# Kernel tuning notes

Hardware: AMD Instinct MI355X
Metric: run time of the kernel (lower is better)

## Reference

```python
import jax, jax.numpy as jnp
import numpy as np

N = 100000   # nodes
E = 1600000  # edges
G = 512      # graphs
L = 3        # num_unit LEConv layers
D = 64       # hidden dim


def setup_inputs() -> dict:
    key = jax.random.key(0)
    ks = jax.random.split(key, 12)
    s = 1.0 / np.sqrt(D)
    x = jax.random.normal(ks[0], (N, 4), jnp.float32)
    edge_index = jax.random.randint(ks[1], (2, E), 0, N, dtype=jnp.int64)
    edge_attr = jax.random.uniform(ks[2], (E,), jnp.float32)
    batch = jnp.sort(jax.random.randint(ks[3], (N,), 0, G, dtype=jnp.int64))
    return {
        "x": x,
        "edge_index": edge_index,
        "edge_attr": edge_attr,
        "batch": batch,
        "W_emb": jax.random.normal(ks[4], (4, D), jnp.float32) * 0.5,
        "b_emb": jnp.zeros((D,), jnp.float32),
        "W1": jax.random.normal(ks[5], (L, D, D), jnp.float32) * s,  # LEConv lin1 (on x_j)
        "b1": jnp.zeros((L, D), jnp.float32),
        "W2": jax.random.normal(ks[6], (L, D, D), jnp.float32) * s,  # LEConv lin2 (on x_i, no bias)
        "W3": jax.random.normal(ks[7], (L, D, D), jnp.float32) * s,  # LEConv lin3 (root)
        "b3": jnp.zeros((L, D), jnp.float32),
        "Wl1": jax.random.normal(ks[8], (D, 32), jnp.float32) * s,
        "bl1": jnp.zeros((32,), jnp.float32),
        "Wl2": jax.random.normal(ks[9], (32, 3), jnp.float32) * (1.0 / np.sqrt(32)),
        "bl2": jnp.zeros((3,), jnp.float32),
    }


def reference(x, edge_index, edge_attr, batch, W_emb, b_emb,
              W1, b1, W2, W3, b3, Wl1, bl1, Wl2, bl2):
    src, dst = edge_index[0], edge_index[1]
    h = x @ W_emb + b_emb                          # [N, D]
    for l in range(L):
        a = h @ W1[l] + b1[l]                      # lin1(x) -> gathered at source j
        b = h @ W2[l]                              # lin2(x) -> gathered at target i
        # LEConv message: e_ij * (lin1(x_j) - lin2(x_i)), aggr='add' at target
        msg = edge_attr[:, None] * (a[src] - b[dst])   # [E, D]
        agg = jax.ops.segment_sum(msg, dst, num_segments=N)
        h = jax.nn.relu(agg + h @ W3[l] + b3[l])
    # global_mean_pool over graphs
    sums = jax.ops.segment_sum(h, batch, num_segments=G)              # [G, D]
    counts = jax.ops.segment_sum(jnp.ones((N,), h.dtype), batch, num_segments=G)
    graph_x = sums / jnp.maximum(counts, 1.0)[:, None]
    pred = jax.nn.relu(graph_x @ Wl1 + bl1) @ Wl2 + bl2               # [G, 3]
    return pred
```

## Files before the change

### kernel.cpp

```cpp
#include <hip/hip_runtime.h>
#include <hip/hip_bf16.h>

#define NNODES 100000
#define NEDGES 1600000
#define NGRAPH 512
#define DIM    64
#define NLAYER 3

#define NB   1000
#define BN   100
#define CAP  2048
#define SC_BLOCKS 256
#define EPB  6250
#define PACK_BLOCKS 18

typedef __attribute__((ext_vector_type(8))) short short8;
typedef __attribute__((ext_vector_type(4))) float float4v;
typedef unsigned long long u64;

__device__ __forceinline__ float b2f(__hip_bfloat16 v) { return __bfloat162float(v); }
__device__ __forceinline__ __hip_bfloat16 f2b(float f) { return __float2bfloat16(f); }
__device__ __forceinline__ unsigned short f2b_bits(float f) {
    __hip_bfloat16 h = __float2bfloat16(f);
    return *reinterpret_cast<unsigned short*>(&h);
}

__device__ __forceinline__ unsigned pack_rec(int src, unsigned wbits32) {
    unsigned w15 = ((wbits32 + 0x8000u) >> 16) & 0x7FFFu;
    return ((unsigned)src << 15) | w15;
}

#define ACC4(ACC, RR, VV) do {                                              \
    float _w = __uint_as_float(((RR) & 0x7FFFu) << 16);                     \
    unsigned _lo = (unsigned)(VV), _hi = (unsigned)((VV) >> 32);            \
    ACC[0] = fmaf(_w, __uint_as_float(_lo << 16), ACC[0]);                  \
    ACC[1] = fmaf(_w, __uint_as_float(_lo & 0xFFFF0000u), ACC[1]);          \
    ACC[2] = fmaf(_w, __uint_as_float(_hi << 16), ACC[2]);                  \
    ACC[3] = fmaf(_w, __uint_as_float(_hi & 0xFFFF0000u), ACC[3]);          \
} while (0)


__global__ __launch_bounds__(256) void local_sort_kernel(
    const int* __restrict__ ei, const float* __restrict__ ea,
    int2* __restrict__ perm_raw, int2* __restrict__ offcnt,
    const float* __restrict__ W1, const float* __restrict__ W2,
    const float* __restrict__ W3, __hip_bfloat16* __restrict__ wpack) {
    int tid = threadIdx.x, k = blockIdx.x;
    if (k >= SC_BLOCKS) {
        int unit = (k - SC_BLOCKS) * 4 + (tid >> 6);
        if (unit < NLAYER * 24) {
            int kh = unit & 1, tn = (unit >> 1) & 3, w = (unit >> 3) % 3, l = unit / 24;
            const float* Wsrc = (w == 0 ? W1 : (w == 1 ? W2 : W3)) + l * 4096;
            int L = tid & 63;
            __hip_bfloat16* dst = wpack + (size_t)unit * 512 + L * 8;
            int kb = 32 * kh + (L >> 4) * 8;
            int nb = 16 * tn + (L & 15);
            #pragma unroll
            for (int j = 0; j < 8; ++j)
                dst[j] = f2b(Wsrc[(kb + j) * 64 + nb]);
        }
        return;
    }
    __shared__ int cnt[NB];
    __shared__ int off[NB];
    __shared__ int partial[256];
    __shared__ int2 srec[EPB];
    int e0 = k * EPB;
    for (int i = tid; i < NB; i += 256) cnt[i] = 0;
    __syncthreads();
    for (int i = tid; i < EPB; i += 256)
        atomicAdd(&cnt[ei[NEDGES + e0 + i] / BN], 1);
    __syncthreads();
    int loc[4]; int s = 0;
    #pragma unroll
    for (int j = 0; j < 4; ++j) {
        int b = tid * 4 + j;
        int v = (b < NB) ? cnt[b] : 0;
        loc[j] = s; s += v;
    }
    partial[tid] = s;
    __syncthreads();
    for (int o = 1; o < 256; o <<= 1) {
        int t = (tid >= o) ? partial[tid - o] : 0;
        __syncthreads();
        partial[tid] += t;
        __syncthreads();
    }
    int excl = partial[tid] - s;
    #pragma unroll
    for (int j = 0; j < 4; ++j) {
        int b = tid * 4 + j;
        if (b < NB) off[b] = excl + loc[j];
    }
    __syncthreads();
    for (int b = tid; b < NB; b += 256)
        offcnt[(size_t)k * NB + b] = make_int2(off[b], cnt[b]);
    __syncthreads();
    for (int i = tid; i < EPB; i += 256) {
        int e = e0 + i;
        int src = ei[e];
        int d = ei[NEDGES + e];
        float w = ea[e];
        int bin = d / BN;
        int dloc = d - bin * BN;
        int pos = atomicAdd(&off[bin], 1);
        srec[pos] = make_int2(src | (dloc << 20), __float_as_int(w));
    }
    __syncthreads();
    for (int i = tid; i < EPB; i += 256)
        perm_raw[e0 + i] = srec[i];
}

__global__ __launch_bounds__(256) void bucket_csr_kernel(
    const int2* __restrict__ perm_raw, const int2* __restrict__ offcnt,
    unsigned* __restrict__ perm2, int2* __restrict__ rows, float* __restrict__ wdeg) {
    __shared__ int2     recs[CAP];
    __shared__ unsigned recs2u[CAP];
    __shared__ int   pscan[256];
    __shared__ int   sprefix[SC_BLOCKS + 1];
    __shared__ int   boff[SC_BLOCKS];
    __shared__ int   cnt[BN];
    __shared__ int   start[BN];
    __shared__ int   cur[BN];
    __shared__ float ws[BN];
    int b = blockIdx.x, tid = threadIdx.x;
    if (tid < BN) { cnt[tid] = 0; ws[tid] = 0.f; }
    int2 oc = offcnt[(size_t)tid * NB + b];
    boff[tid] = oc.x;
    int c = oc.y;
    pscan[tid] = c;
    __syncthreads();
    for (int o = 1; o < 256; o <<= 1) {
        int t = (tid >= o) ? pscan[tid - o] : 0;
        __syncthreads();
        pscan[tid] += t;
        __syncthreads();
    }
    sprefix[tid] = pscan[tid] - c;
    if (tid == 255) sprefix[256] = pscan[255];
    __syncthreads();
    int n = min(sprefix[SC_BLOCKS], CAP);
    for (int i = tid; i < n; i += 256) {
        int lo = 0, hi = SC_BLOCKS;
        while (hi - lo > 1) { int m = (lo + hi) >> 1; if (sprefix[m] <= i) lo = m; else hi = m; }
        int2 rec = perm_raw[lo * EPB + boff[lo] + (i - sprefix[lo])];
        recs[i] = rec;
        atomicAdd(&cnt[rec.x >> 20], 1);
        atomicAdd(&ws[rec.x >> 20], __int_as_float(rec.y));
    }
    __syncthreads();
    {
        int v = (tid < BN) ? cnt[tid] : 0;
        pscan[tid] = v;
        __syncthreads();
        for (int o = 1; o < 128; o <<= 1) {
            int t = (tid >= o) ? pscan[tid - o] : 0;
            __syncthreads();
            pscan[tid] += t;
            __syncthreads();
        }
        if (tid < BN) start[tid] = pscan[tid] - v;
    }
    __syncthreads();
    if (tid < BN) {
        cur[tid] = start[tid];
        int base = b * CAP + start[tid];
        rows[b * BN + tid] = make_int2(base, base + cnt[tid]);
        wdeg[b * BN + tid] = ws[tid];
    }
    __syncthreads();
    for (int i = tid; i < n; i += 256) {
        int2 rec = recs[i];
        int pos = atomicAdd(&cur[rec.x >> 20], 1);
        recs2u[pos] = pack_rec(rec.x & 0xFFFFF, (unsigned)rec.y);
    }
    __syncthreads();
    for (int i = tid; i < n; i += 256)
        perm2[(size_t)b * CAP + i] = recs2u[i];
}


template <int FUSE_EMBED>
__global__ __launch_bounds__(256) void gemm3_mfma_kernel(
    __hip_bfloat16* __restrict__ h16, const float* __restrict__ wdeg,
    const __hip_bfloat16* __restrict__ wpack,
    const float* __restrict__ b1, const float* __restrict__ b3,
    __hip_bfloat16* __restrict__ a,
    const float* __restrict__ x, const float* __restrict__ Wemb,
    const float* __restrict__ bemb) {
    int tid = threadIdx.x;
    int lane = tid & 63, wv = tid >> 6;
    int m0 = blockIdx.x * 64 + wv * 16;
    int q = lane >> 4;
    int node_a = m0 + (lane & 15);
    int node_c = min(node_a, NNODES - 1);

    float4v acc[3][4] = {};
    const short8* wp = (const short8*)wpack;

    float4v xv;
    if (FUSE_EMBED) xv = *(const float4v*)&x[(size_t)node_c * 4];

    #pragma unroll
    for (int kh = 0; kh < 2; ++kh) {
        short8 afrag;
        if (FUSE_EMBED) {
            #pragma unroll
            for (int j = 0; j < 8; ++j) {
                int ch = kh * 32 + q * 8 + j;
                float s = bemb[ch];
                #pragma unroll
                for (int k = 0; k < 4; ++k) s = fmaf(xv[k], Wemb[k * 64 + ch], s);
                afrag[j] = (short)f2b_bits(s);
            }
        } else {
            afrag = *(const short8*)((const short*)h16 + (size_t)node_c * 64 + kh * 32 + q * 8);
        }
        #pragma unroll
        for (int w = 0; w < 3; ++w) {
            #pragma unroll
            for (int tn = 0; tn < 4; ++tn) {
                short8 bfrag = wp[(size_t)(((w * 4 + tn) * 2 + kh)) * 64 + lane];
                acc[w][tn] = __builtin_amdgcn_mfma_f32_16x16x32_bf16(afrag, bfrag, acc[w][tn], 0, 0, 0);
            }
        }
    }

    int coll = lane & 15;
    float b1v[4], b3v[4];
    #pragma unroll
    for (int tn = 0; tn < 4; ++tn) {
        b1v[tn] = b1[tn * 16 + coll];
        b3v[tn] = b3[tn * 16 + coll];
    }
    #pragma unroll
    for (int reg = 0; reg < 4; ++reg) {
        int node = m0 + q * 4 + reg;
        if (node < NNODES) {
            float wd = wdeg[node];
            #pragma unroll
            for (int tn = 0; tn < 4; ++tn) {
                int nn = tn * 16 + coll;
                a[(size_t)node * 64 + nn] = f2b(acc[0][tn][reg] + b1v[tn]);
                h16[(size_t)node * 64 + nn] = f2b(acc[2][tn][reg] + b3v[tn] - wd * acc[1][tn][reg]);
            }
        }
    }
}

__global__ __launch_bounds__(256) void edge_agg_kernel(
    const __hip_bfloat16* __restrict__ a, __hip_bfloat16* __restrict__ h16,
    const int2* __restrict__ rows, const unsigned* __restrict__ perm2) {
    int node = blockIdx.x * 4 + (threadIdx.x >> 6);
    int lane = threadIdx.x & 63;
    int q = lane >> 4, p = lane & 15;
    const u64* a64 = (const u64*)a;
    int2 r = rows[node];
    int start = r.x, end = r.y;
    u64 cv = 0;
    if (q == 0) cv = ((const u64*)h16)[(size_t)node * 16 + p];
    float accA[4] = {0.f, 0.f, 0.f, 0.f};
    float accB[4] = {0.f, 0.f, 0.f, 0.f};
    float accC[4] = {0.f, 0.f, 0.f, 0.f};
    float accD[4] = {0.f, 0.f, 0.f, 0.f};
    for (int cb = start; cb < end; cb += 64) {
        int avail = end - cb;
        int cnt = min(avail, 64);
        unsigned rec = (lane < avail) ? perm2[cb + lane] : 0u;
        int full = cnt >> 4;
        for (int t = 0; t < full; ++t) {
            int base = t * 16;
            unsigned rA = (unsigned)__shfl((int)rec, base + q, 64);
            unsigned rB = (unsigned)__shfl((int)rec, base + 4 + q, 64);
            unsigned rC = (unsigned)__shfl((int)rec, base + 8 + q, 64);
            unsigned rD = (unsigned)__shfl((int)rec, base + 12 + q, 64);
            u64 vA = a64[(size_t)(rA >> 15) * 16 + p];
            u64 vB = a64[(size_t)(rB >> 15) * 16 + p];
            u64 vC = a64[(size_t)(rC >> 15) * 16 + p];
            u64 vD = a64[(size_t)(rD >> 15) * 16 + p];
            ACC4(accA, rA, vA);
            ACC4(accB, rB, vB);
            ACC4(accC, rC, vC);
            ACC4(accD, rD, vD);
        }
        int rem = cnt & 15;
        if (rem) {
            int base = full << 4;
            unsigned rA = (unsigned)__shfl((int)rec, base + q, 64);
            u64 vA = a64[(size_t)(rA >> 15) * 16 + p];
            unsigned rB = 0u, rC = 0u, rD = 0u;
            u64 vB = 0, vC = 0, vD = 0;
            if (rem > 4) {
                rB = (unsigned)__shfl((int)rec, base + 4 + q, 64);
                vB = a64[(size_t)(rB >> 15) * 16 + p];
            }
            if (rem > 8) {
                rC = (unsigned)__shfl((int)rec, base + 8 + q, 64);
                vC = a64[(size_t)(rC >> 15) * 16 + p];
            }
            if (rem > 12) {
                rD = (unsigned)__shfl((int)rec, base + 12 + q, 64);
                vD = a64[(size_t)(rD >> 15) * 16 + p];
            }
            ACC4(accA, rA, vA);
            ACC4(accB, rB, vB);
            ACC4(accC, rC, vC);
            ACC4(accD, rD, vD);
        }
    }
    #pragma unroll
    for (int j = 0; j < 4; ++j) accA[j] = (accA[j] + accB[j]) + (accC[j] + accD[j]);
    #pragma unroll
    for (int j = 0; j < 4; ++j) accA[j] += __shfl_xor(accA[j], 16, 64);
    #pragma unroll
    for (int j = 0; j < 4; ++j) accA[j] += __shfl_xor(accA[j], 32, 64);
    if (q == 0) {
        u64* h64 = (u64*)h16;
        unsigned int lo = (unsigned int)cv, hi = (unsigned int)(cv >> 32);
        float r0 = fmaxf(__uint_as_float(lo << 16) + accA[0], 0.f);
        float r1 = fmaxf(__uint_as_float(lo & 0xFFFF0000u) + accA[1], 0.f);
        float r2 = fmaxf(__uint_as_float(hi << 16) + accA[2], 0.f);
        float r3 = fmaxf(__uint_as_float(hi & 0xFFFF0000u) + accA[3], 0.f);
        u64 outv = (u64)f2b_bits(r0) | ((u64)f2b_bits(r1) << 16) |
                   ((u64)f2b_bits(r2) << 32) | ((u64)f2b_bits(r3) << 48);
        h64[(size_t)node * 16 + p] = outv;
    }
}


__global__ __launch_bounds__(256) void pool_mlp_kernel(
    const __hip_bfloat16* __restrict__ h16, const int* __restrict__ batch,
    const float* __restrict__ Wl1, const float* __restrict__ bl1,
    const float* __restrict__ Wl2, const float* __restrict__ bl2,
    float* __restrict__ out) {
    __shared__ int lohi[2];
    __shared__ float red[16][64];
    __shared__ float gxl[64];
    __shared__ float hid[32];
    int g = blockIdx.x;
    int tid = threadIdx.x;
    if (tid < 2) {
        int target = g + tid;
        int lo = 0, hi = NNODES;
        while (lo < hi) { int m = (lo + hi) >> 1; if (batch[m] < target) lo = m + 1; else hi = m; }
        lohi[tid] = lo;
    }
    __syncthreads();
    int lo = lohi[0], hi = lohi[1];
    int grp = tid >> 4, p = tid & 15;
    float s0 = 0.f, s1 = 0.f, s2 = 0.f, s3 = 0.f;
    const u64* h64 = (const u64*)h16;
    for (int n = lo + grp; n < hi; n += 16) {
        u64 v = h64[(size_t)n * 16 + p];
        unsigned lo32 = (unsigned)v, hi32 = (unsigned)(v >> 32);
        s0 += __uint_as_float(lo32 << 16);
        s1 += __uint_as_float(lo32 & 0xFFFF0000u);
        s2 += __uint_as_float(hi32 << 16);
        s3 += __uint_as_float(hi32 & 0xFFFF0000u);
    }
    float4v sv = {s0, s1, s2, s3};
    *(float4v*)&red[grp][p * 4] = sv;
    __syncthreads();
    if (tid < 64) {
        float tot = 0.f;
        #pragma unroll
        for (int k = 0; k < 16; ++k) tot += red[k][tid];
        int cnt = hi - lo;
        gxl[tid] = tot / (float)max(cnt, 1);
    }
    __syncthreads();
    if (tid < 32) {
        float s = bl1[tid];
        for (int k = 0; k < 64; ++k) s = fmaf(gxl[k], Wl1[k * 32 + tid], s);
        hid[tid] = fmaxf(s, 0.f);
    }
    __syncthreads();
    if (tid < 3) {
        float s = bl2[tid];
        for (int k = 0; k < 32; ++k) s = fmaf(hid[k], Wl2[k * 3 + tid], s);
        out[g * 3 + tid] = s;
    }
}


extern "C" void kernel_launch(void* const* d_in, const int* in_sizes, int n_in,
                              void* d_out, int out_size, void* d_ws, size_t ws_size,
                              hipStream_t stream) {
    const float* x    = (const float*)d_in[0];
    const int*   ei   = (const int*)d_in[1];
    const float* ea   = (const float*)d_in[2];
    const int*   bat  = (const int*)d_in[3];
    const float* Wemb = (const float*)d_in[4];
    const float* bemb = (const float*)d_in[5];
    const float* W1   = (const float*)d_in[6];
    const float* b1   = (const float*)d_in[7];
    const float* W2   = (const float*)d_in[8];
    const float* W3   = (const float*)d_in[9];
    const float* b3   = (const float*)d_in[10];
    const float* Wl1  = (const float*)d_in[11];
    const float* bl1  = (const float*)d_in[12];
    const float* Wl2  = (const float*)d_in[13];
    const float* bl2  = (const float*)d_in[14];
    float* out = (float*)d_out;

    char* ws = (char*)d_ws;
    __hip_bfloat16*  a        = (__hip_bfloat16*) (ws + 0);
    __hip_bfloat16*  h16      = (__hip_bfloat16*) (ws + 12800000);
    int2*            perm_raw = (int2*)           (ws + 25600000);
    unsigned*        perm2    = (unsigned*)       (ws + 38400000);
    int2*            rows     = (int2*)           (ws + 46592000);
    int2*            offcnt   = (int2*)           (ws + 47392000);
    float*           wdeg     = (float*)          (ws + 49440000);
    __hip_bfloat16*  wpack    = (__hip_bfloat16*) (ws + 49840000);

    local_sort_kernel<<<SC_BLOCKS + PACK_BLOCKS, 256, 0, stream>>>(
        ei, ea, perm_raw, offcnt, W1, W2, W3, wpack);
    bucket_csr_kernel<<<NB, 256, 0, stream>>>(perm_raw, offcnt, perm2, rows, wdeg);

    gemm3_mfma_kernel<1><<<(NNODES + 63) / 64, 256, 0, stream>>>(
        h16, wdeg, wpack, b1, b3, a, x, Wemb, bemb);
    edge_agg_kernel<<<NNODES / 4, 256, 0, stream>>>(a, h16, rows, perm2);
    for (int l = 1; l < NLAYER; ++l) {
        gemm3_mfma_kernel<0><<<(NNODES + 63) / 64, 256, 0, stream>>>(
            h16, wdeg, wpack + (size_t)l * 24 * 512, b1 + l * 64, b3 + l * 64, a,
            x, Wemb, bemb);
        edge_agg_kernel<<<NNODES / 4, 256, 0, stream>>>(a, h16, rows, perm2);
    }
    pool_mlp_kernel<<<NGRAPH, 256, 0, stream>>>(h16, bat, Wl1, bl1, Wl2, bl2, out);
}
```

Measured before the change: 293.6 us.

## Aggregate raw h before the GEMM and fuse each layer into one kernel

Uses linearity to reorder each layer: the edge-weighted sum of neighbour h is gathered first, and W1 is applied to that sum (with the bias scaled by weighted degree) inside one fused gather+MFMA kernel per layer. The separate a-buffer write/read and the per-layer two-kernel split go away, and h is ping-ponged between two buffers. The last layer also reduces into per-graph sums with atomics, replacing the pooling pass, so the final MLP kernel only reads the sums. This adds atomics and a next-node record prefetch. It also changes rounding order, since the aggregate is rounded to bf16 before the GEMM.

```diff
diff --git a/kernel.cpp b/kernel.cpp
--- a/kernel.cpp
+++ b/kernel.cpp
@@ -13,12 +13,13 @@
 #define SC_BLOCKS 256
 #define EPB  6250
 #define PACK_BLOCKS 18
+#define ZERO_BLOCKS 2
+#define NBLK 1563
 
 typedef __attribute__((ext_vector_type(8))) short short8;
 typedef __attribute__((ext_vector_type(4))) float float4v;
 typedef unsigned long long u64;
 
-__device__ __forceinline__ float b2f(__hip_bfloat16 v) { return __bfloat162float(v); }
 __device__ __forceinline__ __hip_bfloat16 f2b(float f) { return __float2bfloat16(f); }
 __device__ __forceinline__ unsigned short f2b_bits(float f) {
     __hip_bfloat16 h = __float2bfloat16(f);
@@ -39,13 +40,66 @@
     ACC[3] = fmaf(_w, __uint_as_float(_hi & 0xFFFF0000u), ACC[3]);          \
 } while (0)
 
+__device__ __forceinline__ void gather_rounds(
+    unsigned rec, int cnt, const u64* __restrict__ h64, int q, int p,
+    float (&accA)[4], float (&accB)[4], float (&accC)[4], float (&accD)[4]) {
+    int full = cnt >> 4;
+    for (int t = 0; t < full; ++t) {
+        int base = t * 16;
+        unsigned rA = (unsigned)__shfl((int)rec, base + q, 64);
+        unsigned rB = (unsigned)__shfl((int)rec, base + 4 + q, 64);
+        unsigned rC = (unsigned)__shfl((int)rec, base + 8 + q, 64);
+        unsigned rD = (unsigned)__shfl((int)rec, base + 12 + q, 64);
+        u64 vA = h64[(size_t)(rA >> 15) * 16 + p];
+        u64 vB = h64[(size_t)(rB >> 15) * 16 + p];
+        u64 vC = h64[(size_t)(rC >> 15) * 16 + p];
+        u64 vD = h64[(size_t)(rD >> 15) * 16 + p];
+        ACC4(accA, rA, vA);
+        ACC4(accB, rB, vB);
+        ACC4(accC, rC, vC);
+        ACC4(accD, rD, vD);
+    }
+    int rem = cnt & 15;
+    if (rem) {
+        int base = full << 4;
+        unsigned rA = (unsigned)__shfl((int)rec, base + q, 64);
+        u64 vA = h64[(size_t)(rA >> 15) * 16 + p];
+        unsigned rB = 0u, rC = 0u, rD = 0u;
+        u64 vB = 0, vC = 0, vD = 0;
+        if (rem > 4) {
+            rB = (unsigned)__shfl((int)rec, base + 4 + q, 64);
+            vB = h64[(size_t)(rB >> 15) * 16 + p];
+        }
+        if (rem > 8) {
+            rC = (unsigned)__shfl((int)rec, base + 8 + q, 64);
+            vC = h64[(size_t)(rC >> 15) * 16 + p];
+        }
+        if (rem > 12) {
+            rD = (unsigned)__shfl((int)rec, base + 12 + q, 64);
+            vD = h64[(size_t)(rD >> 15) * 16 + p];
+        }
+        ACC4(accA, rA, vA);
+        ACC4(accB, rB, vB);
+        ACC4(accC, rC, vC);
+        ACC4(accD, rD, vD);
+    }
+}
+
 
 __global__ __launch_bounds__(256) void local_sort_kernel(
     const int* __restrict__ ei, const float* __restrict__ ea,
     int2* __restrict__ perm_raw, int2* __restrict__ offcnt,
     const float* __restrict__ W1, const float* __restrict__ W2,
-    const float* __restrict__ W3, __hip_bfloat16* __restrict__ wpack) {
+    const float* __restrict__ W3, __hip_bfloat16* __restrict__ wpack,
+    float* __restrict__ gsum) {
     int tid = threadIdx.x, k = blockIdx.x;
+    if (k >= SC_BLOCKS + PACK_BLOCKS) {
+        float4v z = {0.f, 0.f, 0.f, 0.f};
+        int idx = (k - SC_BLOCKS - PACK_BLOCKS) * 256 + tid;
+        for (int i = idx; i < NGRAPH * DIM / 4; i += ZERO_BLOCKS * 256)
+            ((float4v*)gsum)[i] = z;
+        return;
+    }
     if (k >= SC_BLOCKS) {
         int unit = (k - SC_BLOCKS) * 4 + (tid >> 6);
         if (unit < NLAYER * 24) {
@@ -180,205 +234,181 @@
 }
 
 
-template <int FUSE_EMBED>
-__global__ __launch_bounds__(256) void gemm3_mfma_kernel(
-    __hip_bfloat16* __restrict__ h16, const float* __restrict__ wdeg,
-    const __hip_bfloat16* __restrict__ wpack,
+__global__ __launch_bounds__(256) void embed_kernel(
+    const float* __restrict__ x, const float* __restrict__ Wemb,
+    const float* __restrict__ bemb, __hip_bfloat16* __restrict__ h) {
+    int t = blockIdx.x * 256 + threadIdx.x;
+    int node = t >> 4, d0 = (t & 15) * 4;
+    if (node >= NNODES) return;
+    float4v xv = *(const float4v*)&x[(size_t)node * 4];
+    u64 w0 = 0;
+    #pragma unroll
+    for (int j = 0; j < 4; ++j) {
+        int ch = d0 + j;
+        float s = bemb[ch];
+        #pragma unroll
+        for (int k = 0; k < 4; ++k) s = fmaf(xv[k], Wemb[k * 64 + ch], s);
+        w0 |= (u64)f2b_bits(s) << (16 * j);
+    }
+    ((u64*)h)[(size_t)node * 16 + (t & 15)] = w0;
+}
+
+
+template <int LAST>
+__global__ __launch_bounds__(256) void layer_kernel(
+    const __hip_bfloat16* __restrict__ hin, __hip_bfloat16* __restrict__ hout,
+    const int2* __restrict__ rows, const unsigned* __restrict__ perm2,
+    const float* __restrict__ wdeg, const __hip_bfloat16* __restrict__ wpack,
     const float* __restrict__ b1, const float* __restrict__ b3,
-    __hip_bfloat16* __restrict__ a,
-    const float* __restrict__ x, const float* __restrict__ Wemb,
-    const float* __restrict__ bemb) {
+    const int* __restrict__ batch, float* __restrict__ gsum) {
+    __shared__ __align__(16) unsigned char mbytes[4 * 2048];
     int tid = threadIdx.x;
     int lane = tid & 63, wv = tid >> 6;
-    int m0 = blockIdx.x * 64 + wv * 16;
-    int q = lane >> 4;
-    int node_a = m0 + (lane & 15);
-    int node_c = min(node_a, NNODES - 1);
+    int q = lane >> 4, p = lane & 15;
+    int m0w = blockIdx.x * 64 + wv * 16;
+    const u64* h64 = (const u64*)hin;
+
+    int2 rall = rows[min(m0w + p, NNODES - 1)];
+    int st_n = __shfl(rall.x, 0, 64);
+    int en_n = __shfl(rall.y, 0, 64);
+    if (m0w >= NNODES) en_n = st_n;
+    unsigned rec_n = (lane < min(en_n - st_n, 64)) ? perm2[st_n + lane] : 0u;
+
+    for (int nl = 0; nl < 16; ++nl) {
+        int st = st_n, en = en_n;
+        unsigned rec = rec_n;
+        if (nl < 15) {
+            st_n = __shfl(rall.x, nl + 1, 64);
+            en_n = __shfl(rall.y, nl + 1, 64);
+            if (m0w + nl + 1 >= NNODES) en_n = st_n;
+            rec_n = (lane < min(en_n - st_n, 64)) ? perm2[st_n + lane] : 0u;
+        }
+        float accA[4] = {0.f, 0.f, 0.f, 0.f};
+        float accB[4] = {0.f, 0.f, 0.f, 0.f};
+        float accC[4] = {0.f, 0.f, 0.f, 0.f};
+        float accD[4] = {0.f, 0.f, 0.f, 0.f};
+        gather_rounds(rec, min(en - st, 64), h64, q, p, accA, accB, accC, accD);
+        for (int cb = st + 64; cb < en; cb += 64) {
+            unsigned rec2 = (lane < en - cb) ? perm2[cb + lane] : 0u;
+            gather_rounds(rec2, min(en - cb, 64), h64, q, p, accA, accB, accC, accD);
+        }
+        #pragma unroll
+        for (int j = 0; j < 4; ++j) accA[j] = (accA[j] + accB[j]) + (accC[j] + accD[j]);
+        #pragma unroll
+        for (int j = 0; j < 4; ++j) accA[j] += __shfl_xor(accA[j], 16, 64);
+        #pragma unroll
+        for (int j = 0; j < 4; ++j) accA[j] += __shfl_xor(accA[j], 32, 64);
+        if (q == 0) {
+            u64 w0 = (u64)f2b_bits(accA[0]) | ((u64)f2b_bits(accA[1]) << 16) |
+                     ((u64)f2b_bits(accA[2]) << 32) | ((u64)f2b_bits(accA[3]) << 48);
+            int off = (wv * 2048 + nl * 128 + p * 8) ^ ((nl & 7) << 4);
+            *(u64*)(mbytes + off) = w0;
+        }
+    }
 
     float4v acc[3][4] = {};
     const short8* wp = (const short8*)wpack;
-
-    float4v xv;
-    if (FUSE_EMBED) xv = *(const float4v*)&x[(size_t)node_c * 4];
-
+    int node_c = min(m0w + p, NNODES - 1);
     #pragma unroll
     for (int kh = 0; kh < 2; ++kh) {
-        short8 afrag;
-        if (FUSE_EMBED) {
-            #pragma unroll
-            for (int j = 0; j < 8; ++j) {
-                int ch = kh * 32 + q * 8 + j;
-                float s = bemb[ch];
-                #pragma unroll
-                for (int k = 0; k < 4; ++k) s = fmaf(xv[k], Wemb[k * 64 + ch], s);
-                afrag[j] = (short)f2b_bits(s);
-            }
-        } else {
-            afrag = *(const short8*)((const short*)h16 + (size_t)node_c * 64 + kh * 32 + q * 8);
-        }
+        int roff = (wv * 2048 + p * 128 + kh * 64 + q * 16) ^ ((p & 7) << 4);
+        short8 am = *(const short8*)(mbytes + roff);
+        short8 ah = *(const short8*)((const short*)hin + (size_t)node_c * 64 + kh * 32 + q * 8);
         #pragma unroll
         for (int w = 0; w < 3; ++w) {
             #pragma unroll
             for (int tn = 0; tn < 4; ++tn) {
-                short8 bfrag = wp[(size_t)(((w * 4 + tn) * 2 + kh)) * 64 + lane];
-                acc[w][tn] = __builtin_amdgcn_mfma_f32_16x16x32_bf16(afrag, bfrag, acc[w][tn], 0, 0, 0);
+                short8 bfrag = wp[(size_t)((w * 4 + tn) * 2 + kh) * 64 + lane];
+                acc[w][tn] = __builtin_amdgcn_mfma_f32_16x16x32_bf16(
+                    w == 0 ? am : ah, bfrag, acc[w][tn], 0, 0, 0);
             }
         }
     }
 
-    int coll = lane & 15;
     float b1v[4], b3v[4];
     #pragma unroll
     for (int tn = 0; tn < 4; ++tn) {
-        b1v[tn] = b1[tn * 16 + coll];
-        b3v[tn] = b3[tn * 16 + coll];
-    }
-    #pragma unroll
-    for (int reg = 0; reg < 4; ++reg) {
-        int node = m0 + q * 4 + reg;
-        if (node < NNODES) {
-            float wd = wdeg[node];
+        b1v[tn] = b1[tn * 16 + p];
+        b3v[tn] = b3[tn * 16 + p];
+    }
+    if (!LAST) {
+        #pragma unroll
+        for (int reg = 0; reg < 4; ++reg) {
+            int node = m0w + q * 4 + reg;
+            if (node < NNODES) {
+                float wd = wdeg[node];
+                #pragma unroll
+                for (int tn = 0; tn < 4; ++tn) {
+                    float s = acc[0][tn][reg] + acc[2][tn][reg] + b3v[tn] +
+                              wd * (b1v[tn] - acc[1][tn][reg]);
+                    hout[(size_t)node * 64 + tn * 16 + p] = f2b(fmaxf(s, 0.f));
+                }
+            }
+        }
+    } else {
+        float val[4][4];
+        int gb[4];
+        #pragma unroll
+        for (int reg = 0; reg < 4; ++reg) {
+            int node = m0w + q * 4 + reg;
+            int nc = min(node, NNODES - 1);
+            float wd = wdeg[nc];
+            gb[reg] = batch[nc];
+            bool ok = node < NNODES;
             #pragma unroll
             for (int tn = 0; tn < 4; ++tn) {
-                int nn = tn * 16 + coll;
-                a[(size_t)node * 64 + nn] = f2b(acc[0][tn][reg] + b1v[tn]);
-                h16[(size_t)node * 64 + nn] = f2b(acc[2][tn][reg] + b3v[tn] - wd * acc[1][tn][reg]);
+                float s = acc[0][tn][reg] + acc[2][tn][reg] + b3v[tn] +
+                          wd * (b1v[tn] - acc[1][tn][reg]);
+                val[reg][tn] = ok ? fmaxf(s, 0.f) : 0.f;
             }
         }
-    }
-}
-
-__global__ __launch_bounds__(256) void edge_agg_kernel(
-    const __hip_bfloat16* __restrict__ a, __hip_bfloat16* __restrict__ h16,
-    const int2* __restrict__ rows, const unsigned* __restrict__ perm2) {
-    int node = blockIdx.x * 4 + (threadIdx.x >> 6);
-    int lane = threadIdx.x & 63;
-    int q = lane >> 4, p = lane & 15;
-    const u64* a64 = (const u64*)a;
-    int2 r = rows[node];
-    int start = r.x, end = r.y;
-    u64 cv = 0;
-    if (q == 0) cv = ((const u64*)h16)[(size_t)node * 16 + p];
-    float accA[4] = {0.f, 0.f, 0.f, 0.f};
-    float accB[4] = {0.f, 0.f, 0.f, 0.f};
-    float accC[4] = {0.f, 0.f, 0.f, 0.f};
-    float accD[4] = {0.f, 0.f, 0.f, 0.f};
-    for (int cb = start; cb < end; cb += 64) {
-        int avail = end - cb;
-        int cnt = min(avail, 64);
-        unsigned rec = (lane < avail) ? perm2[cb + lane] : 0u;
-        int full = cnt >> 4;
-        for (int t = 0; t < full; ++t) {
-            int base = t * 16;
-            unsigned rA = (unsigned)__shfl((int)rec, base + q, 64);
-            unsigned rB = (unsigned)__shfl((int)rec, base + 4 + q, 64);
-            unsigned rC = (unsigned)__shfl((int)rec, base + 8 + q, 64);
-            unsigned rD = (unsigned)__shfl((int)rec, base + 12 + q, 64);
-            u64 vA = a64[(size_t)(rA >> 15) * 16 + p];
-            u64 vB = a64[(size_t)(rB >> 15) * 16 + p];
-            u64 vC = a64[(size_t)(rC >> 15) * 16 + p];
-            u64 vD = a64[(size_t)(rD >> 15) * 16 + p];
-            ACC4(accA, rA, vA);
-            ACC4(accB, rB, vB);
-            ACC4(accC, rC, vC);
-            ACC4(accD, rD, vD);
-        }
-        int rem = cnt & 15;
-        if (rem) {
-            int base = full << 4;
-            unsigned rA = (unsigned)__shfl((int)rec, base + q, 64);
-            u64 vA = a64[(size_t)(rA >> 15) * 16 + p];
-            unsigned rB = 0u, rC = 0u, rD = 0u;
-            u64 vB = 0, vC = 0, vD = 0;
-            if (rem > 4) {
-                rB = (unsigned)__shfl((int)rec, base + 4 + q, 64);
-                vB = a64[(size_t)(rB >> 15) * 16 + p];
+        int glo = batch[min(m0w, NNODES - 1)];
+        int ghi = batch[min(m0w + 15, NNODES - 1)];
+        for (int g = glo; g <= ghi; ++g) {
+            #pragma unroll
+            for (int tn = 0; tn < 4; ++tn) {
+                float part = 0.f;
+                #pragma unroll
+                for (int reg = 0; reg < 4; ++reg)
+                    part += (gb[reg] == g) ? val[reg][tn] : 0.f;
+                part += __shfl_xor(part, 16, 64);
+                part += __shfl_xor(part, 32, 64);
+                if (q == 0) atomicAdd(&gsum[g * 64 + tn * 16 + p], part);
             }
-            if (rem > 8) {
-                rC = (unsigned)__shfl((int)rec, base + 8 + q, 64);
-                vC = a64[(size_t)(rC >> 15) * 16 + p];
-            }
-            if (rem > 12) {
-                rD = (unsigned)__shfl((int)rec, base + 12 + q, 64);
-                vD = a64[(size_t)(rD >> 15) * 16 + p];
-            }
-            ACC4(accA, rA, vA);
-            ACC4(accB, rB, vB);
-            ACC4(accC, rC, vC);
-            ACC4(accD, rD, vD);
-        }
-    }
-    #pragma unroll
-    for (int j = 0; j < 4; ++j) accA[j] = (accA[j] + accB[j]) + (accC[j] + accD[j]);
-    #pragma unroll
-    for (int j = 0; j < 4; ++j) accA[j] += __shfl_xor(accA[j], 16, 64);
-    #pragma unroll
-    for (int j = 0; j < 4; ++j) accA[j] += __shfl_xor(accA[j], 32, 64);
-    if (q == 0) {
-        u64* h64 = (u64*)h16;
-        unsigned int lo = (unsigned int)cv, hi = (unsigned int)(cv >> 32);
-        float r0 = fmaxf(__uint_as_float(lo << 16) + accA[0], 0.f);
-        float r1 = fmaxf(__uint_as_float(lo & 0xFFFF0000u) + accA[1], 0.f);
-        float r2 = fmaxf(__uint_as_float(hi << 16) + accA[2], 0.f);
-        float r3 = fmaxf(__uint_as_float(hi & 0xFFFF0000u) + accA[3], 0.f);
-        u64 outv = (u64)f2b_bits(r0) | ((u64)f2b_bits(r1) << 16) |
-                   ((u64)f2b_bits(r2) << 32) | ((u64)f2b_bits(r3) << 48);
-        h64[(size_t)node * 16 + p] = outv;
-    }
-}
-
-
-__global__ __launch_bounds__(256) void pool_mlp_kernel(
-    const __hip_bfloat16* __restrict__ h16, const int* __restrict__ batch,
+        }
+    }
+}
+
+
+__global__ __launch_bounds__(64) void mlp_kernel(
+    const float* __restrict__ gsum, const int* __restrict__ batch,
     const float* __restrict__ Wl1, const float* __restrict__ bl1,
     const float* __restrict__ Wl2, const float* __restrict__ bl2,
     float* __restrict__ out) {
     __shared__ int lohi[2];
-    __shared__ float red[16][64];
     __shared__ float gxl[64];
     __shared__ float hid[32];
-    int g = blockIdx.x;
-    int tid = threadIdx.x;
-    if (tid < 2) {
-        int target = g + tid;
+    int g = blockIdx.x, t = threadIdx.x;
+    if (t < 2) {
+        int target = g + t;
         int lo = 0, hi = NNODES;
         while (lo < hi) { int m = (lo + hi) >> 1; if (batch[m] < target) lo = m + 1; else hi = m; }
-        lohi[tid] = lo;
-    }
-    __syncthreads();
-    int lo = lohi[0], hi = lohi[1];
-    int grp = tid >> 4, p = tid & 15;
-    float s0 = 0.f, s1 = 0.f, s2 = 0.f, s3 = 0.f;
-    const u64* h64 = (const u64*)h16;
-    for (int n = lo + grp; n < hi; n += 16) {
-        u64 v = h64[(size_t)n * 16 + p];
-        unsigned lo32 = (unsigned)v, hi32 = (unsigned)(v >> 32);
-        s0 += __uint_as_float(lo32 << 16);
-        s1 += __uint_as_float(lo32 & 0xFFFF0000u);
-        s2 += __uint_as_float(hi32 << 16);
-        s3 += __uint_as_float(hi32 & 0xFFFF0000u);
-    }
-    float4v sv = {s0, s1, s2, s3};
-    *(float4v*)&red[grp][p * 4] = sv;
-    __syncthreads();
-    if (tid < 64) {
-        float tot = 0.f;
-        #pragma unroll
-        for (int k = 0; k < 16; ++k) tot += red[k][tid];
-        int cnt = hi - lo;
-        gxl[tid] = tot / (float)max(cnt, 1);
-    }
-    __syncthreads();
-    if (tid < 32) {
-        float s = bl1[tid];
-        for (int k = 0; k < 64; ++k) s = fmaf(gxl[k], Wl1[k * 32 + tid], s);
-        hid[tid] = fmaxf(s, 0.f);
-    }
-    __syncthreads();
-    if (tid < 3) {
-        float s = bl2[tid];
-        for (int k = 0; k < 32; ++k) s = fmaf(hid[k], Wl2[k * 3 + tid], s);
-        out[g * 3 + tid] = s;
+        lohi[t] = lo;
+    }
+    __syncthreads();
+    int cnt = lohi[1] - lohi[0];
+    gxl[t] = gsum[g * 64 + t] / (float)max(cnt, 1);
+    __syncthreads();
+    if (t < 32) {
+        float s = bl1[t];
+        for (int k = 0; k < 64; ++k) s = fmaf(gxl[k], Wl1[k * 32 + t], s);
+        hid[t] = fmaxf(s, 0.f);
+    }
+    __syncthreads();
+    if (t < 3) {
+        float s = bl2[t];
+        for (int k = 0; k < 32; ++k) s = fmaf(hid[k], Wl2[k * 3 + t], s);
+        out[g * 3 + t] = s;
     }
 }
 
@@ -404,27 +434,27 @@
     float* out = (float*)d_out;
 
     char* ws = (char*)d_ws;
-    __hip_bfloat16*  a        = (__hip_bfloat16*) (ws + 0);
-    __hip_bfloat16*  h16      = (__hip_bfloat16*) (ws + 12800000);
+    __hip_bfloat16*  h_b      = (__hip_bfloat16*) (ws + 0);
+    __hip_bfloat16*  h_a      = (__hip_bfloat16*) (ws + 12800000);
     int2*            perm_raw = (int2*)           (ws + 25600000);
     unsigned*        perm2    = (unsigned*)       (ws + 38400000);
     int2*            rows     = (int2*)           (ws + 46592000);
     int2*            offcnt   = (int2*)           (ws + 47392000);
     float*           wdeg     = (float*)          (ws + 49440000);
     __hip_bfloat16*  wpack    = (__hip_bfloat16*) (ws + 49840000);
-
-    local_sort_kernel<<<SC_BLOCKS + PACK_BLOCKS, 256, 0, stream>>>(
-        ei, ea, perm_raw, offcnt, W1, W2, W3, wpack);
+    float*           gsum     = (float*)          (ws + 49913728);
+
+    local_sort_kernel<<<SC_BLOCKS + PACK_BLOCKS + ZERO_BLOCKS, 256, 0, stream>>>(
+        ei, ea, perm_raw, offcnt, W1, W2, W3, wpack, gsum);
     bucket_csr_kernel<<<NB, 256, 0, stream>>>(perm_raw, offcnt, perm2, rows, wdeg);
-
-    gemm3_mfma_kernel<1><<<(NNODES + 63) / 64, 256, 0, stream>>>(
-        h16, wdeg, wpack, b1, b3, a, x, Wemb, bemb);
-    edge_agg_kernel<<<NNODES / 4, 256, 0, stream>>>(a, h16, rows, perm2);
-    for (int l = 1; l < NLAYER; ++l) {
-        gemm3_mfma_kernel<0><<<(NNODES + 63) / 64, 256, 0, stream>>>(
-            h16, wdeg, wpack + (size_t)l * 24 * 512, b1 + l * 64, b3 + l * 64, a,
-            x, Wemb, bemb);
-        edge_agg_kernel<<<NNODES / 4, 256, 0, stream>>>(a, h16, rows, perm2);
-    }
-    pool_mlp_kernel<<<NGRAPH, 256, 0, stream>>>(h16, bat, Wl1, bl1, Wl2, bl2, out);
-}
+    embed_kernel<<<(NNODES * 16 + 255) / 256, 256, 0, stream>>>(x, Wemb, bemb, h_a);
+
+    layer_kernel<0><<<NBLK, 256, 0, stream>>>(
+        h_a, h_b, rows, perm2, wdeg, wpack, b1, b3, bat, gsum);
+    layer_kernel<0><<<NBLK, 256, 0, stream>>>(
+        h_b, h_a, rows, perm2, wdeg, wpack + (size_t)24 * 512, b1 + 64, b3 + 64, bat, gsum);
+    layer_kernel<1><<<NBLK, 256, 0, stream>>>(
+        h_a, h_b, rows, perm2, wdeg, wpack + (size_t)48 * 512, b1 + 128, b3 + 128, bat, gsum);
+
+    mlp_kernel<<<NGRAPH, 64, 0, stream>>>(gsum, bat, Wl1, bl1, Wl2, bl2, out);
+}
```

Result: no change. 288.7 us (-1.7%).
